# Performance work log

Measured on AMD Instinct MI355X. Metric: run time of the kernel, lower is better.

## Reference

```python
import jax, jax.numpy as jnp
import numpy as np

B, C, H, W = 8, 64, 64, 64
OUT_H, OUT_W = 32, 32


def setup_inputs() -> dict:
    key = jax.random.key(0)
    ks = jax.random.split(key, 9)
    s = 1.0 / np.sqrt(C).astype(np.float32)
    return {
        "x": jax.random.normal(ks[0], (B, C, H, W), jnp.float32),
        "wq": jax.random.normal(ks[1], (C, C), jnp.float32) * s,
        "bq": jax.random.normal(ks[2], (C,), jnp.float32) * 0.01,
        "wk": jax.random.normal(ks[3], (C, C), jnp.float32) * s,
        "bk": jax.random.normal(ks[4], (C,), jnp.float32) * 0.01,
        "wv": jax.random.normal(ks[5], (C, C), jnp.float32) * s,
        "bv": jax.random.normal(ks[6], (C,), jnp.float32) * 0.01,
        "wm": jax.random.normal(ks[7], (C, C), jnp.float32) * s,
        "bm": jax.random.normal(ks[8], (C,), jnp.float32) * 0.01,
    }


def reference(x, wq, bq, wk, bk, wv, bv, wm, bm):
    # pushforward: self-attention over spatial tokens, 1x1-conv mixing + ReLU,
    # then bilinear resize to out_shape (align_corners=False semantics).
    b, c, h, w = x.shape
    t = x.reshape(b, c, h * w).transpose(0, 2, 1)  # [B, HW, C] tokens
    q = jnp.einsum('bnc,dc->bnd', t, wq) + bq      # 1x1 conv == per-pixel linear
    k = jnp.einsum('bnc,dc->bnd', t, wk) + bk
    v = jnp.einsum('bnc,dc->bnd', t, wv) + bv
    scores = jnp.einsum('bnc,bmc->bnm', q, k) / jnp.sqrt(jnp.float32(c))  # [B, HW, HW]
    attn = jax.nn.softmax(scores, axis=-1)
    o = jnp.einsum('bnm,bmc->bnc', attn, v)        # [B, HW, C]
    mixed = jax.nn.relu(jnp.einsum('bnc,dc->bnd', o, wm) + bm)
    out = mixed.transpose(0, 2, 1).reshape(b, c, h, w)
    # F.interpolate(mode='bilinear', align_corners=False) == half-pixel bilinear, no antialias
    out = jax.image.resize(out, (b, c, OUT_H, OUT_W), method='bilinear', antialias=False)
    return out
```

## Files before the change

kernel.cpp:

```cpp
#include <hip/hip_runtime.h>
#include <stdint.h>

typedef unsigned short u16;
typedef unsigned int   u32;
typedef __attribute__((ext_vector_type(8)))  short short8;
typedef __attribute__((ext_vector_type(4)))  float f32x4;
typedef __attribute__((ext_vector_type(16))) float f32x16;

#define NTOK 4096
#define LOG2E 1.44269504088896340736f
#define QS    (0.125f * LOG2E)

__device__ __forceinline__ u16 f2bf(float f) {
    u32 u = __builtin_bit_cast(u32, f);
    u += 0x7fffu + ((u >> 16) & 1u);
    return (u16)(u >> 16);
}
__device__ __forceinline__ float bf2f(u16 v) {
    return __builtin_bit_cast(float, (u32)v << 16);
}
__device__ __forceinline__ u32 pk_hu(float a, float b) {
    u32 ua = __builtin_bit_cast(u32, a) + 0x8000u;
    u32 ub = __builtin_bit_cast(u32, b) + 0x8000u;
    return __builtin_amdgcn_perm(ub, ua, 0x07060302);
}
__device__ __forceinline__ f32x16 zero16() {
    f32x16 v;
#pragma unroll
    for (int i = 0; i < 16; ++i) v[i] = 0.f;
    return v;
}

#define MFMA16x32 __builtin_amdgcn_mfma_f32_16x16x32_bf16
#define MFMA32x16 __builtin_amdgcn_mfma_f32_32x32x16_bf16

__global__ __launch_bounds__(256) void qkv_mfma4(
    const float* __restrict__ x,
    const float* __restrict__ wq, const float* __restrict__ bq,
    const float* __restrict__ wk, const float* __restrict__ bk,
    const float* __restrict__ wv, const float* __restrict__ bv,
    u16* __restrict__ Q, u16* __restrict__ K, u16* __restrict__ Vp)
{
    __shared__ __align__(16) u16 Wl[3 * 64 * 72];
    __shared__ __align__(16) u16 Xl[64 * 64];
    const int tid  = threadIdx.x;
    const int b    = blockIdx.x & 7;
    const int slab = blockIdx.x >> 3;
    const int n0   = slab << 6;
    const int wave = tid >> 6;
    const int lane = tid & 63;
    const int quad = lane >> 4;
    const int l15  = lane & 15;

#pragma unroll
    for (int j = 0; j < 12; ++j) {
        const float* src = (j < 4) ? wq : (j < 8) ? wk : wv;
        const float sc = (j < 4) ? QS : 1.0f;
        const int idx = (j & 3) * 1024 + tid * 4;
        const float4 v = *(const float4*)(src + idx);
        uint2 pk;
        pk.x = (u32)f2bf(v.x * sc) | ((u32)f2bf(v.y * sc) << 16);
        pk.y = (u32)f2bf(v.z * sc) | ((u32)f2bf(v.w * sc) << 16);
        *(uint2*)&Wl[(j >> 2) * 4608 + (idx >> 6) * 72 + (idx & 63)] = pk;
    }

    float4 xs[4];
#pragma unroll
    for (int g = 0; g < 4; ++g) {
        const int ch = g * 16 + wave * 4 + quad;
        xs[g] = *(const float4*)(x + ((size_t)(b * 64 + ch)) * NTOK + n0 + l15 * 4);
    }
#pragma unroll
    for (int g = 0; g < 4; ++g) {
        const int ch = g * 16 + wave * 4 + quad;
        const float vv[4] = {xs[g].x, xs[g].y, xs[g].z, xs[g].w};
#pragma unroll
        for (int e = 0; e < 4; ++e) {
            const int tok = l15 * 4 + e;
            Xl[tok * 64 + (((ch >> 3) ^ (tok & 7)) & 7) * 8 + (ch & 7)] = f2bf(vv[e]);
        }
    }
    __syncthreads();

    const int row0 = wave * 16 + l15;
    short8 xf[2];
#pragma unroll
    for (int kk = 0; kk < 2; ++kk)
        xf[kk] = *(const short8*)&Xl[row0 * 64 + (((kk * 4 + quad) ^ (row0 & 7)) & 7) * 8];

    const size_t tokbase = (size_t)b * NTOK + n0 + wave * 16;

#pragma unroll
    for (int mat = 0; mat < 2; ++mat) {
        const float* bias = (mat == 0) ? bq : bk;
        const float bsc = (mat == 0) ? QS : 1.0f;
#pragma unroll
        for (int mt = 0; mt < 4; ++mt) {
            const u16* wr = &Wl[mat * 4608 + (mt * 16 + l15) * 72 + quad * 8];
            const short8 wf0 = *(const short8*)(wr);
            const short8 wf1 = *(const short8*)(wr + 32);
            f32x4 acc = {0.f, 0.f, 0.f, 0.f};
            acc = MFMA16x32(wf0, xf[0], acc, 0, 0, 0);
            acc = MFMA16x32(wf1, xf[1], acc, 0, 0, 0);
            const float4 b4 = *(const float4*)(bias + mt * 16 + quad * 4);
            uint2 pk;
            pk.x = (u32)f2bf(acc[0] + b4.x * bsc) | ((u32)f2bf(acc[1] + b4.y * bsc) << 16);
            pk.y = (u32)f2bf(acc[2] + b4.z * bsc) | ((u32)f2bf(acc[3] + b4.w * bsc) << 16);
            u16* dst = (mat == 0) ? Q : K;
            *(uint2*)(dst + (tokbase + l15) * 64 + mt * 16 + quad * 4) = pk;
        }
    }

    __syncthreads();
    u16* Vl = Xl;
    const int tok = wave * 16 + l15;
#pragma unroll
    for (int mt = 0; mt < 4; ++mt) {
        const u16* wr = &Wl[2 * 4608 + (mt * 16 + l15) * 72 + quad * 8];
        const short8 wf0 = *(const short8*)(wr);
        const short8 wf1 = *(const short8*)(wr + 32);
        f32x4 acc = {0.f, 0.f, 0.f, 0.f};
        acc = MFMA16x32(wf0, xf[0], acc, 0, 0, 0);
        acc = MFMA16x32(wf1, xf[1], acc, 0, 0, 0);
        const float4 b4 = *(const float4*)(bv + mt * 16 + quad * 4);
        const float o[4] = {acc[0] + b4.x, acc[1] + b4.y, acc[2] + b4.z, acc[3] + b4.w};
#pragma unroll
        for (int r = 0; r < 4; ++r) {
            const int d = mt * 16 + quad * 4 + r;
            Vl[d * 64 + (((tok >> 3) ^ ((d >> 1) & 7)) & 7) * 8 + (tok & 7)] = f2bf(o[r]);
        }
    }
    __syncthreads();

#pragma unroll
    for (int dd = 0; dd < 4; ++dd) {
        const int d2   = (tid >> 4) + dd * 16;
        const int tok0 = (tid & 15) * 4;
        const int slot = ((tok0 >> 3) ^ ((d2 >> 1) & 7)) & 7;
        const uint2 v2 = *(const uint2*)&Vl[d2 * 64 + slot * 8 + (tok0 & 7)];
        const int gt = slab * 2 + (tok0 >> 5);
        *(uint2*)(Vp + (((size_t)b * 128 + gt) * 64 + d2) * 32 + (tok0 & 31)) = v2;
    }
}

__global__ __launch_bounds__(512, 2) void attn7(
    const u16* __restrict__ Q, const u16* __restrict__ K,
    const u16* __restrict__ Vp,
    const float* __restrict__ wm, const float* __restrict__ bm,
    float* __restrict__ out)
{
    __shared__ __align__(16) char smem[54272];
    const int tid  = threadIdx.x;
    const int wave = tid >> 6;
    const int lane = tid & 63;
    const int c31  = lane & 31;
    const int hw   = lane >> 5;
    const int quad = lane >> 4;
    const int l15  = lane & 15;
    const int h    = wave >> 2;
    const int s    = wave & 3;
    const int b    = blockIdx.x & 7;
    const int oh   = blockIdx.x >> 3;
    const int n0   = oh * 128;

    short8 qf[2][4];
#pragma unroll
    for (int nt = 0; nt < 2; ++nt)
#pragma unroll
        for (int ks = 0; ks < 4; ++ks)
            qf[nt][ks] = *(const short8*)(Q + ((size_t)(b * NTOK + n0 + h * 64 + nt * 32 + c31)) * 64
                                            + ks * 16 + hw * 8);

    const u16* Kb  = K + ((size_t)b * NTOK + s * 1024) * 64;
    const u16* Vbp = Vp + ((size_t)b * 128 + s * 32) * 2048;

    f32x16 O[2][2];
#pragma unroll
    for (int mt = 0; mt < 2; ++mt)
#pragma unroll
        for (int nt = 0; nt < 2; ++nt) O[mt][nt] = zero16();
    float lpa[2] = {0.f, 0.f};

    auto load_kv = [&](short8 (&kf)[4], short8 (&vf)[4], int t) {
        const int tc = (t < 32) ? t : 31;
        const u16* kt = Kb + (size_t)tc * 2048;
#pragma unroll
        for (int ks = 0; ks < 4; ++ks)
            kf[ks] = *(const short8*)(kt + c31 * 64 + ks * 16 + hw * 8);
        const u16* vt = Vbp + (size_t)tc * 2048;
#pragma unroll
        for (int mk = 0; mk < 4; ++mk)
            vf[mk] = *(const short8*)(vt + ((mk >> 1) * 32 + c31) * 32 + (mk & 1) * 16 + hw * 8);
    };

    auto tile_tail = [&](const f32x16 (&sv)[2], const short8 (&vf)[4]) {
#pragma unroll
        for (int nt = 0; nt < 2; ++nt) {
            float p[16];
#pragma unroll
            for (int r = 0; r < 16; ++r) p[r] = __builtin_amdgcn_exp2f(sv[nt][r]);
            lpa[nt] += (((p[0] + p[1]) + (p[2] + p[3])) + ((p[4] + p[5]) + (p[6] + p[7])))
                     + (((p[8] + p[9]) + (p[10] + p[11])) + ((p[12] + p[13]) + (p[14] + p[15])));
            u32 g[8];
#pragma unroll
            for (int gi = 0; gi < 8; ++gi) g[gi] = pk_hu(p[2 * gi], p[2 * gi + 1]);
            const u32 rA = __shfl_xor(hw ? g[0] : g[2], 32);
            const u32 rB = __shfl_xor(hw ? g[1] : g[3], 32);
            const u32 rC = __shfl_xor(hw ? g[4] : g[6], 32);
            const u32 rD = __shfl_xor(hw ? g[5] : g[7], 32);
            uint4 B0, B1;
            B0.x = hw ? rA : g[0];  B0.y = hw ? rB : g[1];
            B0.z = hw ? g[2] : rA;  B0.w = hw ? g[3] : rB;
            B1.x = hw ? rC : g[4];  B1.y = hw ? rD : g[5];
            B1.z = hw ? g[6] : rC;  B1.w = hw ? g[7] : rD;
            const short8 pb0 = __builtin_bit_cast(short8, B0);
            const short8 pb1 = __builtin_bit_cast(short8, B1);
            O[0][nt] = MFMA32x16(vf[0], pb0, O[0][nt], 0, 0, 0);
            O[0][nt] = MFMA32x16(vf[1], pb1, O[0][nt], 0, 0, 0);
            O[1][nt] = MFMA32x16(vf[2], pb0, O[1][nt], 0, 0, 0);
            O[1][nt] = MFMA32x16(vf[3], pb1, O[1][nt], 0, 0, 0);
        }
    };

    short8 kfA[4], vfA[4], kfB[4], vfB[4];
    load_kv(kfA, vfA, 0);

#pragma unroll 1
    for (int tt = 0; tt < 16; ++tt) {
        const int t0 = tt * 2;
        f32x16 sv0[2];
#pragma unroll
        for (int nt = 0; nt < 2; ++nt) {
            f32x16 a = zero16();
            a = MFMA32x16(kfA[0], qf[nt][0], a, 0, 0, 0);
            a = MFMA32x16(kfA[1], qf[nt][1], a, 0, 0, 0);
            a = MFMA32x16(kfA[2], qf[nt][2], a, 0, 0, 0);
            a = MFMA32x16(kfA[3], qf[nt][3], a, 0, 0, 0);
            sv0[nt] = a;
        }
        load_kv(kfB, vfB, t0 + 1);
        tile_tail(sv0, vfA);

        f32x16 sv1[2];
#pragma unroll
        for (int nt = 0; nt < 2; ++nt) {
            f32x16 a = zero16();
            a = MFMA32x16(kfB[0], qf[nt][0], a, 0, 0, 0);
            a = MFMA32x16(kfB[1], qf[nt][1], a, 0, 0, 0);
            a = MFMA32x16(kfB[2], qf[nt][2], a, 0, 0, 0);
            a = MFMA32x16(kfB[3], qf[nt][3], a, 0, 0, 0);
            sv1[nt] = a;
        }
        load_kv(kfA, vfA, t0 + 2);
        tile_tail(sv1, vfB);
    }

#pragma unroll
    for (int nt = 0; nt < 2; ++nt) lpa[nt] += __shfl_xor(lpa[nt], 32);

    float* lpbuf = (float*)(smem + 52224);
    if (hw == 0) {
#pragma unroll
        for (int nt = 0; nt < 2; ++nt)
            lpbuf[(h * 4 + s) * 64 + nt * 32 + c31] = lpa[nt];
    }
    if (s != 0) {
        u16* sec = (u16*)smem + (h * 3 + s - 1) * 4352;
#pragma unroll
        for (int mt = 0; mt < 2; ++mt)
#pragma unroll
            for (int nt = 0; nt < 2; ++nt)
#pragma unroll
                for (int r = 0; r < 16; ++r) {
                    const int ch = mt * 32 + (r & 3) + 8 * (r >> 2) + 4 * hw;
                    sec[(nt * 32 + c31) * 68 + ch] = f2bf(O[mt][nt][r]);
                }
    }
    __syncthreads();

    float rinv[2];
    if (s == 0) {
#pragma unroll
        for (int nt = 0; nt < 2; ++nt) {
            float sum = 0.f;
#pragma unroll
            for (int sx = 0; sx < 4; ++sx)
                sum += lpbuf[(h * 4 + sx) * 64 + nt * 32 + c31];
            rinv[nt] = 1.0f / sum;
        }
#pragma unroll
        for (int sx = 1; sx < 4; ++sx) {
            const u16* sec = (const u16*)smem + (h * 3 + sx - 1) * 4352;
#pragma unroll
            for (int mt = 0; mt < 2; ++mt)
#pragma unroll
                for (int nt = 0; nt < 2; ++nt)
#pragma unroll
                    for (int r = 0; r < 16; ++r) {
                        const int ch = mt * 32 + (r & 3) + 8 * (r >> 2) + 4 * hw;
                        O[mt][nt][r] += bf2f(sec[(nt * 32 + c31) * 68 + ch]);
                    }
        }
    }
    short8 wB[4][2];
    float bb[4];
#pragma unroll
    for (int nt = 0; nt < 4; ++nt) {
        const int d = nt * 16 + l15;
        const float* wr = wm + (size_t)d * 64 + quad * 8;
        const float4 a0 = *(const float4*)(wr);
        const float4 a1 = *(const float4*)(wr + 4);
        const float4 c0 = *(const float4*)(wr + 32);
        const float4 c1 = *(const float4*)(wr + 36);
        ((u32*)&wB[nt][0])[0] = pk_hu(a0.y, a0.x) ^ 0u, ((u32*)&wB[nt][0])[0] = (u32)f2bf(a0.x) | ((u32)f2bf(a0.y) << 16);
        ((u32*)&wB[nt][0])[1] = (u32)f2bf(a0.z) | ((u32)f2bf(a0.w) << 16);
        ((u32*)&wB[nt][0])[2] = (u32)f2bf(a1.x) | ((u32)f2bf(a1.y) << 16);
        ((u32*)&wB[nt][0])[3] = (u32)f2bf(a1.z) | ((u32)f2bf(a1.w) << 16);
        ((u32*)&wB[nt][1])[0] = (u32)f2bf(c0.x) | ((u32)f2bf(c0.y) << 16);
        ((u32*)&wB[nt][1])[1] = (u32)f2bf(c0.z) | ((u32)f2bf(c0.w) << 16);
        ((u32*)&wB[nt][1])[2] = (u32)f2bf(c1.x) | ((u32)f2bf(c1.y) << 16);
        ((u32*)&wB[nt][1])[3] = (u32)f2bf(c1.z) | ((u32)f2bf(c1.w) << 16);
        bb[nt] = bm[d];
    }
    __syncthreads();

    if (s == 0) {
        u16* M0 = (u16*)smem + h * 4096;
#pragma unroll
        for (int mt = 0; mt < 2; ++mt)
#pragma unroll
            for (int nt = 0; nt < 2; ++nt)
#pragma unroll
                for (int r = 0; r < 16; ++r) {
                    const int lr = nt * 32 + c31;
                    const int ch = mt * 32 + (r & 3) + 8 * (r >> 2) + 4 * hw;
                    const float v = O[mt][nt][r] * rinv[nt];
                    M0[lr * 64 + (((ch >> 3) ^ (lr & 7)) & 7) * 8 + (ch & 7)] = f2bf(v);
                }
    }
    __syncthreads();

    const u16* M0r = (const u16*)smem + (wave >> 2) * 4096;
    const int lr = (wave & 3) * 16 + l15;
    const short8 af0 = *(const short8*)&M0r[lr * 64 + ((quad ^ (lr & 7)) & 7) * 8];
    const short8 af1 = *(const short8*)&M0r[lr * 64 + (((4 + quad) ^ (lr & 7)) & 7) * 8];
    float* Mf = (float*)(smem + 16384);
#pragma unroll
    for (int nt = 0; nt < 4; ++nt) {
        f32x4 acc = {0.f, 0.f, 0.f, 0.f};
        acc = MFMA16x32(af0, wB[nt][0], acc, 0, 0, 0);
        acc = MFMA16x32(af1, wB[nt][1], acc, 0, 0, 0);
#pragma unroll
        for (int r = 0; r < 4; ++r) {
            float v = acc[r] + bb[nt];
            v = v > 0.f ? v : 0.f;
            Mf[(wave * 16 + quad * 4 + r) * 68 + nt * 16 + l15] = v;
        }
    }
    __syncthreads();

    const int ow = tid & 31;
    const int cb = (tid >> 5) & 15;
#pragma unroll
    for (int i = 0; i < 4; ++i) {
        const int c = cb + i * 16;
        const float v = 0.25f * (Mf[(2 * ow) * 68 + c] + Mf[(2 * ow + 1) * 68 + c]
                               + Mf[(64 + 2 * ow) * 68 + c] + Mf[(65 + 2 * ow) * 68 + c]);
        out[((size_t)(b * 64 + c) * 32 + oh) * 32 + ow] = v;
    }
}

extern "C" void kernel_launch(void* const* d_in, const int* in_sizes, int n_in,
                              void* d_out, int out_size, void* d_ws, size_t ws_size,
                              hipStream_t stream) {
    (void)in_sizes; (void)n_in; (void)out_size; (void)ws_size;
    const float* x  = (const float*)d_in[0];
    const float* wq = (const float*)d_in[1];
    const float* bq = (const float*)d_in[2];
    const float* wk = (const float*)d_in[3];
    const float* bk = (const float*)d_in[4];
    const float* wv = (const float*)d_in[5];
    const float* bv = (const float*)d_in[6];
    const float* wm = (const float*)d_in[7];
    const float* bm = (const float*)d_in[8];

    u16* Q  = (u16*)d_ws;
    u16* K  = Q + (size_t)8 * NTOK * 64;
    u16* Vp = K + (size_t)8 * NTOK * 64;

    qkv_mfma4<<<512, 256, 0, stream>>>(x, wq, bq, wk, bk, wv, bv, Q, K, Vp);
    attn7<<<256, 512, 0, stream>>>(Q, K, Vp, wm, bm, (float*)d_out);
}
```

Baseline: 135.7 us.

## Permute V token layout to drop P shuffles and software-pipeline S compute

The QKV kernel now writes V with tokens permuted within each 32-token group, swapping bits 2 and 3 of the token index. This makes the MFMA output layout of P match the B-operand layout directly, so the cross-half-wave shuffles and selects in the softmax tail go away. The attention loop is also restructured so that the next tile's QK^T MFMAs are issued before the current tile's exp/PV work, with K/V loads two tiles ahead. The cost is more live registers (two score sets plus two K/V fragment sets) under the 512x2 launch bound, and the loop now loads tiles up to index 33, which are clamped to 31.

```diff
diff --git a/kernel.cpp b/kernel.cpp
--- a/kernel.cpp
+++ b/kernel.cpp
@@ -138,12 +138,14 @@
         const int tok0 = (tid & 15) * 4;
         const int slot = ((tok0 >> 3) ^ ((d2 >> 1) & 7)) & 7;
         const uint2 v2 = *(const uint2*)&Vl[d2 * 64 + slot * 8 + (tok0 & 7)];
-        const int gt = slab * 2 + (tok0 >> 5);
-        *(uint2*)(Vp + (((size_t)b * 128 + gt) * 64 + d2) * 32 + (tok0 & 31)) = v2;
-    }
-}
-
-__global__ __launch_bounds__(512, 2) void attn7(
+        const int gt  = slab * 2 + (tok0 >> 5);
+        const int tl  = tok0 & 31;
+        const int sl  = (tl & 0x13) | (((tl >> 2) & 1) << 3) | (((tl >> 3) & 1) << 2);
+        *(uint2*)(Vp + (((size_t)b * 128 + gt) * 64 + d2) * 32 + sl) = v2;
+    }
+}
+
+__global__ __launch_bounds__(512, 2) void attn8(
     const u16* __restrict__ Q, const u16* __restrict__ K,
     const u16* __restrict__ Vp,
     const float* __restrict__ wm, const float* __restrict__ bm,
@@ -193,6 +195,18 @@
             vf[mk] = *(const short8*)(vt + ((mk >> 1) * 32 + c31) * 32 + (mk & 1) * 16 + hw * 8);
     };
 
+    auto S_compute = [&](f32x16 (&sv)[2], const short8 (&kf)[4]) {
+#pragma unroll
+        for (int nt = 0; nt < 2; ++nt) {
+            f32x16 a = zero16();
+            a = MFMA32x16(kf[0], qf[nt][0], a, 0, 0, 0);
+            a = MFMA32x16(kf[1], qf[nt][1], a, 0, 0, 0);
+            a = MFMA32x16(kf[2], qf[nt][2], a, 0, 0, 0);
+            a = MFMA32x16(kf[3], qf[nt][3], a, 0, 0, 0);
+            sv[nt] = a;
+        }
+    };
+
     auto tile_tail = [&](const f32x16 (&sv)[2], const short8 (&vf)[4]) {
 #pragma unroll
         for (int nt = 0; nt < 2; ++nt) {
@@ -201,18 +215,11 @@
             for (int r = 0; r < 16; ++r) p[r] = __builtin_amdgcn_exp2f(sv[nt][r]);
             lpa[nt] += (((p[0] + p[1]) + (p[2] + p[3])) + ((p[4] + p[5]) + (p[6] + p[7])))
                      + (((p[8] + p[9]) + (p[10] + p[11])) + ((p[12] + p[13]) + (p[14] + p[15])));
-            u32 g[8];
-#pragma unroll
-            for (int gi = 0; gi < 8; ++gi) g[gi] = pk_hu(p[2 * gi], p[2 * gi + 1]);
-            const u32 rA = __shfl_xor(hw ? g[0] : g[2], 32);
-            const u32 rB = __shfl_xor(hw ? g[1] : g[3], 32);
-            const u32 rC = __shfl_xor(hw ? g[4] : g[6], 32);
-            const u32 rD = __shfl_xor(hw ? g[5] : g[7], 32);
             uint4 B0, B1;
-            B0.x = hw ? rA : g[0];  B0.y = hw ? rB : g[1];
-            B0.z = hw ? g[2] : rA;  B0.w = hw ? g[3] : rB;
-            B1.x = hw ? rC : g[4];  B1.y = hw ? rD : g[5];
-            B1.z = hw ? g[6] : rC;  B1.w = hw ? g[7] : rD;
+            B0.x = pk_hu(p[0],  p[1]);  B0.y = pk_hu(p[2],  p[3]);
+            B0.z = pk_hu(p[4],  p[5]);  B0.w = pk_hu(p[6],  p[7]);
+            B1.x = pk_hu(p[8],  p[9]);  B1.y = pk_hu(p[10], p[11]);
+            B1.z = pk_hu(p[12], p[13]); B1.w = pk_hu(p[14], p[15]);
             const short8 pb0 = __builtin_bit_cast(short8, B0);
             const short8 pb1 = __builtin_bit_cast(short8, B1);
             O[0][nt] = MFMA32x16(vf[0], pb0, O[0][nt], 0, 0, 0);
@@ -223,36 +230,20 @@
     };
 
     short8 kfA[4], vfA[4], kfB[4], vfB[4];
+    f32x16 svA[2], svB[2];
     load_kv(kfA, vfA, 0);
+    load_kv(kfB, vfB, 1);
+    S_compute(svA, kfA);
 
 #pragma unroll 1
     for (int tt = 0; tt < 16; ++tt) {
         const int t0 = tt * 2;
-        f32x16 sv0[2];
-#pragma unroll
-        for (int nt = 0; nt < 2; ++nt) {
-            f32x16 a = zero16();
-            a = MFMA32x16(kfA[0], qf[nt][0], a, 0, 0, 0);
-            a = MFMA32x16(kfA[1], qf[nt][1], a, 0, 0, 0);
-            a = MFMA32x16(kfA[2], qf[nt][2], a, 0, 0, 0);
-            a = MFMA32x16(kfA[3], qf[nt][3], a, 0, 0, 0);
-            sv0[nt] = a;
-        }
-        load_kv(kfB, vfB, t0 + 1);
-        tile_tail(sv0, vfA);
-
-        f32x16 sv1[2];
-#pragma unroll
-        for (int nt = 0; nt < 2; ++nt) {
-            f32x16 a = zero16();
-            a = MFMA32x16(kfB[0], qf[nt][0], a, 0, 0, 0);
-            a = MFMA32x16(kfB[1], qf[nt][1], a, 0, 0, 0);
-            a = MFMA32x16(kfB[2], qf[nt][2], a, 0, 0, 0);
-            a = MFMA32x16(kfB[3], qf[nt][3], a, 0, 0, 0);
-            sv1[nt] = a;
-        }
+        S_compute(svB, kfB);
+        tile_tail(svA, vfA);
         load_kv(kfA, vfA, t0 + 2);
-        tile_tail(sv1, vfB);
+        S_compute(svA, kfA);
+        tile_tail(svB, vfB);
+        load_kv(kfB, vfB, t0 + 3);
     }
 
 #pragma unroll
@@ -312,7 +303,7 @@
         const float4 a1 = *(const float4*)(wr + 4);
         const float4 c0 = *(const float4*)(wr + 32);
         const float4 c1 = *(const float4*)(wr + 36);
-        ((u32*)&wB[nt][0])[0] = pk_hu(a0.y, a0.x) ^ 0u, ((u32*)&wB[nt][0])[0] = (u32)f2bf(a0.x) | ((u32)f2bf(a0.y) << 16);
+        ((u32*)&wB[nt][0])[0] = (u32)f2bf(a0.x) | ((u32)f2bf(a0.y) << 16);
         ((u32*)&wB[nt][0])[1] = (u32)f2bf(a0.z) | ((u32)f2bf(a0.w) << 16);
         ((u32*)&wB[nt][0])[2] = (u32)f2bf(a1.x) | ((u32)f2bf(a1.y) << 16);
         ((u32*)&wB[nt][0])[3] = (u32)f2bf(a1.z) | ((u32)f2bf(a1.w) << 16);
@@ -389,5 +380,5 @@
     u16* Vp = K + (size_t)8 * NTOK * 64;
 
     qkv_mfma4<<<512, 256, 0, stream>>>(x, wq, bq, wk, bk, wv, bv, Q, K, Vp);
-    attn7<<<256, 512, 0, stream>>>(Q, K, Vp, wm, bm, (float*)d_out);
-}
+    attn8<<<256, 512, 0, stream>>>(Q, K, Vp, wm, bm, (float*)d_out);
+}
```

Result: no change. 136.2 us (+0.4%).
